# Performance work log

Measured on AMD Instinct MI355X. Metric: run time of the kernel, lower is better.

Reference implementation:

```python
import jax, jax.numpy as jnp
import numpy as np

EPS = 1e-7


def setup_inputs() -> dict:
    key = jax.random.key(0)
    k1, k2, k3 = jax.random.split(key, 3)
    N = 4194304
    risk_scores = jax.random.normal(k1, (N,), dtype=jnp.float32)
    times = jax.random.randint(k2, (N,), 0, 50000, dtype=jnp.int32)
    events = jax.random.randint(k3, (N,), 0, 2, dtype=jnp.int32)
    return {"risk_scores": risk_scores, "times": times, "events": events}


def _efron_loss(risk_scores, times, events):
    N = risk_scores.shape[0]
    # sort descending by time (stable), as in torch.argsort(times, descending=True)
    order = jnp.argsort(-times, stable=True)
    lr = risk_scores[order]          # log risk, sorted
    t = times[order]
    e = events[order]
    risk = jnp.exp(lr)
    # reversed cumsum: risk set sum for each position (suffix sum)
    csr = jnp.cumsum(risk[::-1])[::-1]
    m = (e == 1)
    mf = m.astype(lr.dtype)
    # segment id per unique time value (contiguous after sort)
    boundary = jnp.concatenate([jnp.zeros((1,), jnp.int32),
                                (t[1:] != t[:-1]).astype(jnp.int32)])
    seg = jnp.cumsum(boundary)       # [N] in [0, N)
    idx = jnp.arange(N)
    # per-segment stats over events
    n_per_seg = jax.ops.segment_sum(mf, seg, num_segments=N)            # n_events at this time
    risk_at_seg = jax.ops.segment_sum(risk * mf, seg, num_segments=N)   # sum of exp(lr) over tied events
    first_ev = jax.ops.segment_min(jnp.where(m, idx, N), seg, num_segments=N)  # event_idx[0]
    seg_start = jax.ops.segment_min(idx, seg, num_segments=N)
    # within-tie event rank j (0-based): events in this segment strictly before i
    c_excl = jnp.cumsum(mf) - mf
    j = c_excl - c_excl[seg_start[seg]]
    n_i = n_per_seg[seg]
    risk_time_i = risk_at_seg[seg]
    risk_set_i = csr[jnp.clip(first_ev[seg], 0, N - 1)]
    correction = (j / jnp.maximum(n_i, 1.0)) * risk_time_i
    per_event = jnp.log(risk_set_i - correction + EPS) - lr
    total_loss = jnp.sum(jnp.where(m, per_event, 0.0))
    total_events = jnp.sum(mf)
    return jnp.where(total_events > 0, total_loss / jnp.maximum(total_events, 1.0), 0.0)


def reference(risk_scores, times, events):
    return _efron_loss(risk_scores, times, events)
```

## Files before the change

kernel.cpp:

```cpp
#include <hip/hip_runtime.h>
#include <math.h>

#define TBINS   50000
#define NR      5
#define RBINS   10000
#define GROUP   256
#define NGROUPS 196
#define EPSF    1e-7f
#define PTHR    1024
#define STRIDE  (PTHR * 8)
#define MAXNS   104
#define MAXNB   (NR * 128)

#define OFF_ALLG  0
#define OFF_EVG   200000
#define OFF_CNTG  400000
#define OFF_GSUM  600000
#define OFF_SCAL  600800
#define OFF_NEV   600816
#define OFF_LRP   600832
#define OFF_NP    603392
#define OFF_SLICE 605952
#define PER_SLICE 400000

__global__ __launch_bounds__(PTHR, 8) void k_pass(
        const float* __restrict__ lr, const int* __restrict__ tm,
        const int* __restrict__ ev, int N, int NS, int CH, char* ws) {
    __shared__ float    s_all[RBINS];
    __shared__ unsigned s_evcnt[RBINS];
    __shared__ float    red_f[16];
    __shared__ int      red_i[16];

    int bid = blockIdx.x;
    int range, slice;
    if ((NS & 7) == 0) {
        int x  = bid & 7;
        int q  = bid >> 3;
        range  = q % NR;
        slice  = (q / NR) * 8 + x;
    } else {
        range = bid % NR;
        slice = bid / NR;
    }
    int rbase = range * RBINS;
    int tid   = threadIdx.x;

    for (int i = tid; i < RBINS; i += PTHR) { s_all[i] = 0.f; s_evcnt[i] = 0u; }
    __syncthreads();

    float l_lr = 0.f;
    int   l_n  = 0;
    int begin = slice * CH;
    int end   = begin + CH; if (end > N) end = N;
    int span  = end - begin; if (span < 0) span = 0;
    int jmax  = span / STRIDE;

    const float* plr = lr + begin + tid * 8;
    const int*   ptm = tm + begin + tid * 8;
    const int*   pev = ev + begin + tid * 8;

#define PROC1(T, L, E) {                                                  \
        unsigned rel_ = (unsigned)((T) - rbase);                          \
        if (rel_ < (unsigned)RBINS) {                                     \
            float r_ = __expf(L);                                         \
            atomicAdd(&s_all[rel_], r_);                                  \
            if ((E) != 0) {                                               \
                l_lr += (L); l_n++;                                       \
                unsigned enc_ = (1u << 28) + (unsigned)(r_ * 65536.0f + 0.5f); \
                atomicAdd(&s_evcnt[rel_], enc_);                          \
            }                                                             \
        } }

#define PROC8(TA, TB, LA, LB, EA, EB)                                    \
        PROC1(TA.x, LA.x, EA.x) PROC1(TA.y, LA.y, EA.y)                  \
        PROC1(TA.z, LA.z, EA.z) PROC1(TA.w, LA.w, EA.w)                  \
        PROC1(TB.x, LB.x, EB.x) PROC1(TB.y, LB.y, EB.y)                  \
        PROC1(TB.z, LB.z, EB.z) PROC1(TB.w, LB.w, EB.w)

#define LOADSLOT(TA, TB, LA, LB, EA, EB, OFF)                            \
        TA = *(const int4*)(ptm + (OFF));   TB = *(const int4*)(ptm + (OFF) + 4); \
        LA = *(const float4*)(plr + (OFF)); LB = *(const float4*)(plr + (OFF) + 4); \
        EA = *(const int4*)(pev + (OFF));   EB = *(const int4*)(pev + (OFF) + 4);

    int4 ta0, tb0, ea0, eb0; float4 la0, lb0;
    int4 ta1, tb1, ea1, eb1; float4 la1, lb1;
    if (jmax > 0) { LOADSLOT(ta0, tb0, la0, lb0, ea0, eb0, 0) }
    if (jmax > 1) { LOADSLOT(ta1, tb1, la1, lb1, ea1, eb1, STRIDE) }

    for (int j = 0; j < jmax; j += 2) {
        PROC8(ta0, tb0, la0, lb0, ea0, eb0)
        if (j + 2 < jmax) { int off = (j + 2) * STRIDE; LOADSLOT(ta0, tb0, la0, lb0, ea0, eb0, off) }
        if (j + 1 < jmax) {
            PROC8(ta1, tb1, la1, lb1, ea1, eb1)
            if (j + 3 < jmax) { int off = (j + 3) * STRIDE; LOADSLOT(ta1, tb1, la1, lb1, ea1, eb1, off) }
        }
    }
    for (int i = begin + jmax * STRIDE + tid; i < end; i += PTHR) {
        int T = tm[i]; float L = lr[i]; int E = ev[i];
        PROC1(T, L, E)
    }

    int lane = tid & 63, wv = tid >> 6;
    #pragma unroll
    for (int off = 32; off > 0; off >>= 1) {
        l_lr += __shfl_down(l_lr, off, 64);
        l_n  += __shfl_down(l_n,  off, 64);
    }
    if (lane == 0) { red_f[wv] = l_lr; red_i[wv] = l_n; }
    __syncthreads();
    if (tid == 0) {
        float s = 0.f; int c = 0;
        #pragma unroll
        for (int w = 0; w < 16; ++w) { s += red_f[w]; c += red_i[w]; }
        ((float*)(ws + OFF_LRP))[bid] = s;
        ((int*)(ws + OFF_NP))[bid]   = c;
    }

    float*    wa  = (float*)(ws + OFF_SLICE + (size_t)slice * PER_SLICE);
    unsigned* wec = (unsigned*)(ws + OFF_SLICE + (size_t)slice * PER_SLICE + (size_t)TBINS * 4);
    for (int i = tid; i < RBINS; i += PTHR) {
        wa[rbase + i]  = s_all[i];
        wec[rbase + i] = s_evcnt[i];
    }
}

__global__ __launch_bounds__(256) void k_reduce(char* ws, int NS, int NB,
                                                float* all_g, float* ev_g, int* cnt_g,
                                                float* gsum, double* scal, int* nev) {
    __shared__ float lds[4];
    __shared__ float ldsf2[4];
    __shared__ int   ldsi2[4];
    int tid = threadIdx.x;
    int b = blockIdx.x * 256 + tid;
    float a = 0.f, d = 0.f; int c = 0;
    if (b < TBINS) {
        const char* base = ws + OFF_SLICE;
        for (int s = 0; s < NS; ++s) {
            const float*    wa  = (const float*)(base + (size_t)s * PER_SLICE);
            const unsigned* wec = (const unsigned*)(base + (size_t)s * PER_SLICE + (size_t)TBINS * 4);
            a += wa[b];
            unsigned e = wec[b];
            c += (int)(e >> 28);
            d += (float)(e & 0x0FFFFFFFu) * (1.0f / 65536.0f);
        }
        all_g[b] = a; ev_g[b] = d; cnt_g[b] = c;
    }
    int lane = tid & 63, wv = tid >> 6;
    float v = a;
    #pragma unroll
    for (int off = 32; off > 0; off >>= 1) v += __shfl_down(v, off, 64);
    if (lane == 0) lds[wv] = v;
    __syncthreads();
    if (tid == 0) {
        float s = 0.f;
        #pragma unroll
        for (int w = 0; w < 4; ++w) s += lds[w];
        gsum[blockIdx.x] = s;
    }

    if (blockIdx.x == 0) {
        float pl = 0.f; int pn = 0;
        for (int i = tid; i < NB; i += 256) {
            pl += ((const float*)(ws + OFF_LRP))[i];
            pn += ((const int*)(ws + OFF_NP))[i];
        }
        #pragma unroll
        for (int off = 32; off > 0; off >>= 1) {
            pl += __shfl_down(pl, off, 64);
            pn += __shfl_down(pn, off, 64);
        }
        if (lane == 0) { ldsf2[wv] = pl; ldsi2[wv] = pn; }
        __syncthreads();
        if (tid == 0) {
            float s = 0.f; int n = 0;
            #pragma unroll
            for (int w = 0; w < 4; ++w) { s += ldsf2[w]; n += ldsi2[w]; }
            scal[0] = (double)s;
            scal[1] = 0.0;
            *nev    = n;
        }
    }
}

__global__ __launch_bounds__(256) void k_loss(
        const float* __restrict__ all_g, const float* __restrict__ gsum,
        const int* __restrict__ cnt_g, const float* __restrict__ ev_g,
        double* scal) {
    __shared__ float lds_r[4];
    __shared__ float lds_s[4];
    __shared__ float sh_base;
    int b   = blockIdx.x;
    int tid = threadIdx.x;
    int t   = b * GROUP + tid;
    int lane = tid & 63, wv = tid >> 6;

    float gv = (tid < b) ? gsum[tid] : 0.f;
    float red = gv;
    #pragma unroll
    for (int off = 32; off > 0; off >>= 1) red += __shfl_down(red, off, 64);
    if (lane == 0) lds_r[wv] = red;
    __syncthreads();
    if (tid == 0) {
        float s = 0.f;
        #pragma unroll
        for (int w = 0; w < 4; ++w) s += lds_r[w];
        sh_base = s;
    }
    __syncthreads();
    float base = sh_base;

    float v = (t < TBINS) ? all_g[t] : 0.f;
    float x = v;
    #pragma unroll
    for (int off = 1; off < 64; off <<= 1) {
        float y = __shfl_up(x, off, 64);
        if (lane >= off) x += y;
    }
    if (lane == 63) lds_s[wv] = x;
    __syncthreads();
    float wbase = 0.f;
    for (int w = 0; w < wv; ++w) wbase += lds_s[w];
    float prefix = base + wbase + (x - v);

    float acc = 0.f;
    if (t < TBINS) {
        int n = cnt_g[t];
        if (n > 0) {
            float D  = ev_g[t];
            float nf = (float)n;
            float P  = D + (v - D) * (nf / (nf + 1.f));
            float R  = prefix + P;
            for (int j = 0; j < n; ++j) {
                float arg = R - ((float)j / nf) * D + EPSF;
                acc += __logf(arg);
            }
        }
    }
    __syncthreads();
    #pragma unroll
    for (int off = 32; off > 0; off >>= 1) acc += __shfl_down(acc, off, 64);
    if (lane == 0) lds_r[wv] = acc;
    __syncthreads();
    if (tid == 0) {
        float s = 0.f;
        #pragma unroll
        for (int w = 0; w < 4; ++w) s += lds_r[w];
        atomicAdd(&scal[1], (double)s);
    }
}

__global__ void k_final(const double* __restrict__ scal,
                        const int* __restrict__ nev, float* out) {
    if (threadIdx.x == 0 && blockIdx.x == 0) {
        int n = *nev;
        double loss = (n > 0) ? (scal[1] - scal[0]) / (double)n : 0.0;
        out[0] = (float)loss;
    }
}

extern "C" void kernel_launch(void* const* d_in, const int* in_sizes, int n_in,
                              void* d_out, int out_size, void* d_ws, size_t ws_size,
                              hipStream_t stream) {
    const float* lr = (const float*)d_in[0];
    const int*   tm = (const int*)d_in[1];
    const int*   ev = (const int*)d_in[2];
    int N = in_sizes[0];

    char*   ws    = (char*)d_ws;
    float*  all_g = (float*)(ws + OFF_ALLG);
    float*  ev_g  = (float*)(ws + OFF_EVG);
    int*    cnt_g = (int*)(ws + OFF_CNTG);
    float*  gsum  = (float*)(ws + OFF_GSUM);
    double* scal  = (double*)(ws + OFF_SCAL);
    int*    nev   = (int*)(ws + OFF_NEV);

    size_t avail = (ws_size > (size_t)OFF_SLICE) ? ws_size - OFF_SLICE : 0;
    int NS = (int)(avail / PER_SLICE);
    if (NS > MAXNS) NS = MAXNS;
    if (NS >= 8) NS &= ~7;
    if (NS < 1) NS = 1;
    int NB = NR * NS;
    int CH = (int)(((long long)N + (long long)NS * STRIDE - 1) / ((long long)NS * STRIDE)) * STRIDE;

    k_pass<<<NB, PTHR, 0, stream>>>(lr, tm, ev, N, NS, CH, ws);
    k_reduce<<<NGROUPS, 256, 0, stream>>>(ws, NS, NB, all_g, ev_g, cnt_g, gsum, scal, nev);
    k_loss<<<NGROUPS, 256, 0, stream>>>(all_g, gsum, cnt_g, ev_g, scal);
    k_final<<<1, 64, 0, stream>>>(scal, nev, (float*)d_out);
}
```

Measured before the change: 93.75 us.

## Pack time, half-precision risk and event flag into one word before histogramming

Adds a prep kernel that reads the three input arrays once, computes exp(lr), and packs the time (high 16 bits), an fp16 risk value and the event bit into one 32-bit word. It also reduces the event log-risk sums there. The histogram pass then rereads only the packed array across its range blocks, with 4 time ranges instead of 5 and at most 64 slices. This cuts redundant global reads and repeated exp work, at the cost of an extra kernel, a packed-array write, and fp16 rounding of risk values that may hurt accuracy.

```diff
diff --git a/kernel.cpp b/kernel.cpp
--- a/kernel.cpp
+++ b/kernel.cpp
@@ -1,16 +1,17 @@
 #include <hip/hip_runtime.h>
+#include <hip/hip_fp16.h>
 #include <math.h>
 
 #define TBINS   50000
-#define NR      5
-#define RBINS   10000
+#define NR      4
+#define RBINS   12500
 #define GROUP   256
 #define NGROUPS 196
 #define EPSF    1e-7f
 #define PTHR    1024
 #define STRIDE  (PTHR * 8)
-#define MAXNS   104
-#define MAXNB   (NR * 128)
+#define MAXNS   64
+#define NPREP   1024
 
 #define OFF_ALLG  0
 #define OFF_EVG   200000
@@ -19,112 +20,142 @@
 #define OFF_SCAL  600800
 #define OFF_NEV   600816
 #define OFF_LRP   600832
-#define OFF_NP    603392
-#define OFF_SLICE 605952
+#define OFF_NP    604928
+#define OFF_PACK  609024
 #define PER_SLICE 400000
 
-__global__ __launch_bounds__(PTHR, 8) void k_pass(
+__global__ __launch_bounds__(256) void k_prep(
         const float* __restrict__ lr, const int* __restrict__ tm,
-        const int* __restrict__ ev, int N, int NS, int CH, char* ws) {
+        const int* __restrict__ ev, int N, unsigned* __restrict__ packed,
+        float* lrp, int* np) {
+    __shared__ float red_f[4];
+    __shared__ int   red_i[4];
+    int tid = threadIdx.x;
+    int gid = blockIdx.x * 256 + tid;
+    const int T = NPREP * 256;
+    float l_lr = 0.f;
+    int   l_n  = 0;
+
+#define PACK1(L, TT, E, OUT) {                                            \
+        float r_ = __expf(L);                                             \
+        unsigned hb_ = (unsigned)__half_as_ushort(__float2half(r_));      \
+        if ((E) != 0) { hb_ |= 0x8000u; l_lr += (L); l_n++; }             \
+        OUT = ((unsigned)(TT) << 16) | hb_; }
+
+    int nvec = N & ~3;
+    for (int base = gid * 4; base < nvec; base += T * 4) {
+        float4 l4 = *(const float4*)(lr + base);
+        int4   t4 = *(const int4*)(tm + base);
+        int4   e4 = *(const int4*)(ev + base);
+        uint4 o;
+        PACK1(l4.x, t4.x, e4.x, o.x)
+        PACK1(l4.y, t4.y, e4.y, o.y)
+        PACK1(l4.z, t4.z, e4.z, o.z)
+        PACK1(l4.w, t4.w, e4.w, o.w)
+        *(uint4*)(packed + base) = o;
+    }
+    for (int i = nvec + gid; i < N; i += T) {
+        unsigned o;
+        PACK1(lr[i], tm[i], ev[i], o)
+        packed[i] = o;
+    }
+
+    int lane = tid & 63, wv = tid >> 6;
+    #pragma unroll
+    for (int off = 32; off > 0; off >>= 1) {
+        l_lr += __shfl_down(l_lr, off, 64);
+        l_n  += __shfl_down(l_n,  off, 64);
+    }
+    if (lane == 0) { red_f[wv] = l_lr; red_i[wv] = l_n; }
+    __syncthreads();
+    if (tid == 0) {
+        float s = 0.f; int c = 0;
+        #pragma unroll
+        for (int w = 0; w < 4; ++w) { s += red_f[w]; c += red_i[w]; }
+        lrp[blockIdx.x] = s;
+        np[blockIdx.x]  = c;
+    }
+}
+
+__global__ __launch_bounds__(PTHR) void k_pass(
+        const unsigned* __restrict__ packed, int N, int NS, int CH, char* slices) {
     __shared__ float    s_all[RBINS];
     __shared__ unsigned s_evcnt[RBINS];
-    __shared__ float    red_f[16];
-    __shared__ int      red_i[16];
 
     int bid = blockIdx.x;
     int range, slice;
     if ((NS & 7) == 0) {
         int x  = bid & 7;
         int q  = bid >> 3;
-        range  = q % NR;
-        slice  = (q / NR) * 8 + x;
+        range  = q & 3;
+        slice  = (q >> 2) * 8 + x;
     } else {
-        range = bid % NR;
-        slice = bid / NR;
-    }
-    int rbase = range * RBINS;
-    int tid   = threadIdx.x;
+        range = bid & 3;
+        slice = bid >> 2;
+    }
+    unsigned rbase = (unsigned)(range * RBINS);
+    int tid = threadIdx.x;
 
     for (int i = tid; i < RBINS; i += PTHR) { s_all[i] = 0.f; s_evcnt[i] = 0u; }
     __syncthreads();
 
-    float l_lr = 0.f;
-    int   l_n  = 0;
     int begin = slice * CH;
     int end   = begin + CH; if (end > N) end = N;
     int span  = end - begin; if (span < 0) span = 0;
     int jmax  = span / STRIDE;
 
-    const float* plr = lr + begin + tid * 8;
-    const int*   ptm = tm + begin + tid * 8;
-    const int*   pev = ev + begin + tid * 8;
-
-#define PROC1(T, L, E) {                                                  \
-        unsigned rel_ = (unsigned)((T) - rbase);                          \
+    const unsigned* pp = packed + begin + tid * 8;
+
+#define PROC1(P) {                                                        \
+        unsigned rel_ = ((P) >> 16) - rbase;                              \
         if (rel_ < (unsigned)RBINS) {                                     \
-            float r_ = __expf(L);                                         \
+            float r_ = __half2float(__ushort_as_half((unsigned short)((P) & 0x7FFFu))); \
             atomicAdd(&s_all[rel_], r_);                                  \
-            if ((E) != 0) {                                               \
-                l_lr += (L); l_n++;                                       \
+            if ((P) & 0x8000u) {                                          \
                 unsigned enc_ = (1u << 28) + (unsigned)(r_ * 65536.0f + 0.5f); \
                 atomicAdd(&s_evcnt[rel_], enc_);                          \
             }                                                             \
         } }
 
-#define PROC8(TA, TB, LA, LB, EA, EB)                                    \
-        PROC1(TA.x, LA.x, EA.x) PROC1(TA.y, LA.y, EA.y)                  \
-        PROC1(TA.z, LA.z, EA.z) PROC1(TA.w, LA.w, EA.w)                  \
-        PROC1(TB.x, LB.x, EB.x) PROC1(TB.y, LB.y, EB.y)                  \
-        PROC1(TB.z, LB.z, EB.z) PROC1(TB.w, LB.w, EB.w)
-
-#define LOADSLOT(TA, TB, LA, LB, EA, EB, OFF)                            \
-        TA = *(const int4*)(ptm + (OFF));   TB = *(const int4*)(ptm + (OFF) + 4); \
-        LA = *(const float4*)(plr + (OFF)); LB = *(const float4*)(plr + (OFF) + 4); \
-        EA = *(const int4*)(pev + (OFF));   EB = *(const int4*)(pev + (OFF) + 4);
-
-    int4 ta0, tb0, ea0, eb0; float4 la0, lb0;
-    int4 ta1, tb1, ea1, eb1; float4 la1, lb1;
-    if (jmax > 0) { LOADSLOT(ta0, tb0, la0, lb0, ea0, eb0, 0) }
-    if (jmax > 1) { LOADSLOT(ta1, tb1, la1, lb1, ea1, eb1, STRIDE) }
+#define PROC8(A, B)                                                      \
+        PROC1(A.x) PROC1(A.y) PROC1(A.z) PROC1(A.w)                      \
+        PROC1(B.x) PROC1(B.y) PROC1(B.z) PROC1(B.w)
+
+    uint4 a0, b0, a1, b1;
+    if (jmax > 0) { a0 = *(const uint4*)pp; b0 = *(const uint4*)(pp + 4); }
+    if (jmax > 1) { a1 = *(const uint4*)(pp + STRIDE); b1 = *(const uint4*)(pp + STRIDE + 4); }
 
     for (int j = 0; j < jmax; j += 2) {
-        PROC8(ta0, tb0, la0, lb0, ea0, eb0)
-        if (j + 2 < jmax) { int off = (j + 2) * STRIDE; LOADSLOT(ta0, tb0, la0, lb0, ea0, eb0, off) }
+        PROC8(a0, b0)
+        if (j + 2 < jmax) {
+            a0 = *(const uint4*)(pp + (j + 2) * STRIDE);
+            b0 = *(const uint4*)(pp + (j + 2) * STRIDE + 4);
+        }
         if (j + 1 < jmax) {
-            PROC8(ta1, tb1, la1, lb1, ea1, eb1)
-            if (j + 3 < jmax) { int off = (j + 3) * STRIDE; LOADSLOT(ta1, tb1, la1, lb1, ea1, eb1, off) }
+            PROC8(a1, b1)
+            if (j + 3 < jmax) {
+                a1 = *(const uint4*)(pp + (j + 3) * STRIDE);
+                b1 = *(const uint4*)(pp + (j + 3) * STRIDE + 4);
+            }
         }
     }
     for (int i = begin + jmax * STRIDE + tid; i < end; i += PTHR) {
-        int T = tm[i]; float L = lr[i]; int E = ev[i];
-        PROC1(T, L, E)
-    }
-
-    int lane = tid & 63, wv = tid >> 6;
-    #pragma unroll
-    for (int off = 32; off > 0; off >>= 1) {
-        l_lr += __shfl_down(l_lr, off, 64);
-        l_n  += __shfl_down(l_n,  off, 64);
-    }
-    if (lane == 0) { red_f[wv] = l_lr; red_i[wv] = l_n; }
-    __syncthreads();
-    if (tid == 0) {
-        float s = 0.f; int c = 0;
-        #pragma unroll
-        for (int w = 0; w < 16; ++w) { s += red_f[w]; c += red_i[w]; }
-        ((float*)(ws + OFF_LRP))[bid] = s;
-        ((int*)(ws + OFF_NP))[bid]   = c;
-    }
-
-    float*    wa  = (float*)(ws + OFF_SLICE + (size_t)slice * PER_SLICE);
-    unsigned* wec = (unsigned*)(ws + OFF_SLICE + (size_t)slice * PER_SLICE + (size_t)TBINS * 4);
+        unsigned P = packed[i];
+        PROC1(P)
+    }
+    __syncthreads();
+
+    float*    wa  = (float*)(slices + (size_t)slice * PER_SLICE);
+    unsigned* wec = (unsigned*)(slices + (size_t)slice * PER_SLICE + (size_t)TBINS * 4);
     for (int i = tid; i < RBINS; i += PTHR) {
         wa[rbase + i]  = s_all[i];
         wec[rbase + i] = s_evcnt[i];
     }
 }
 
-__global__ __launch_bounds__(256) void k_reduce(char* ws, int NS, int NB,
+__global__ __launch_bounds__(256) void k_reduce(const char* __restrict__ slices, int NS,
+                                                const float* __restrict__ lrp,
+                                                const int* __restrict__ np,
                                                 float* all_g, float* ev_g, int* cnt_g,
                                                 float* gsum, double* scal, int* nev) {
     __shared__ float lds[4];
@@ -134,10 +165,9 @@
     int b = blockIdx.x * 256 + tid;
     float a = 0.f, d = 0.f; int c = 0;
     if (b < TBINS) {
-        const char* base = ws + OFF_SLICE;
         for (int s = 0; s < NS; ++s) {
-            const float*    wa  = (const float*)(base + (size_t)s * PER_SLICE);
-            const unsigned* wec = (const unsigned*)(base + (size_t)s * PER_SLICE + (size_t)TBINS * 4);
+            const float*    wa  = (const float*)(slices + (size_t)s * PER_SLICE);
+            const unsigned* wec = (const unsigned*)(slices + (size_t)s * PER_SLICE + (size_t)TBINS * 4);
             a += wa[b];
             unsigned e = wec[b];
             c += (int)(e >> 28);
@@ -160,10 +190,7 @@
 
     if (blockIdx.x == 0) {
         float pl = 0.f; int pn = 0;
-        for (int i = tid; i < NB; i += 256) {
-            pl += ((const float*)(ws + OFF_LRP))[i];
-            pn += ((const int*)(ws + OFF_NP))[i];
-        }
+        for (int i = tid; i < NPREP; i += 256) { pl += lrp[i]; pn += np[i]; }
         #pragma unroll
         for (int off = 32; off > 0; off >>= 1) {
             pl += __shfl_down(pl, off, 64);
@@ -266,15 +293,21 @@
     const int*   ev = (const int*)d_in[2];
     int N = in_sizes[0];
 
-    char*   ws    = (char*)d_ws;
-    float*  all_g = (float*)(ws + OFF_ALLG);
-    float*  ev_g  = (float*)(ws + OFF_EVG);
-    int*    cnt_g = (int*)(ws + OFF_CNTG);
-    float*  gsum  = (float*)(ws + OFF_GSUM);
-    double* scal  = (double*)(ws + OFF_SCAL);
-    int*    nev   = (int*)(ws + OFF_NEV);
-
-    size_t avail = (ws_size > (size_t)OFF_SLICE) ? ws_size - OFF_SLICE : 0;
+    char*     ws     = (char*)d_ws;
+    float*    all_g  = (float*)(ws + OFF_ALLG);
+    float*    ev_g   = (float*)(ws + OFF_EVG);
+    int*      cnt_g  = (int*)(ws + OFF_CNTG);
+    float*    gsum   = (float*)(ws + OFF_GSUM);
+    double*   scal   = (double*)(ws + OFF_SCAL);
+    int*      nev    = (int*)(ws + OFF_NEV);
+    float*    lrp    = (float*)(ws + OFF_LRP);
+    int*      np     = (int*)(ws + OFF_NP);
+    unsigned* packed = (unsigned*)(ws + OFF_PACK);
+
+    size_t off_slice = ((size_t)OFF_PACK + (size_t)N * 4 + 255) & ~(size_t)255;
+    char*  slices    = ws + off_slice;
+
+    size_t avail = (ws_size > off_slice) ? ws_size - off_slice : 0;
     int NS = (int)(avail / PER_SLICE);
     if (NS > MAXNS) NS = MAXNS;
     if (NS >= 8) NS &= ~7;
@@ -282,8 +315,9 @@
     int NB = NR * NS;
     int CH = (int)(((long long)N + (long long)NS * STRIDE - 1) / ((long long)NS * STRIDE)) * STRIDE;
 
-    k_pass<<<NB, PTHR, 0, stream>>>(lr, tm, ev, N, NS, CH, ws);
-    k_reduce<<<NGROUPS, 256, 0, stream>>>(ws, NS, NB, all_g, ev_g, cnt_g, gsum, scal, nev);
+    k_prep<<<NPREP, 256, 0, stream>>>(lr, tm, ev, N, packed, lrp, np);
+    k_pass<<<NB, PTHR, 0, stream>>>(packed, N, NS, CH, slices);
+    k_reduce<<<NGROUPS, 256, 0, stream>>>(slices, NS, lrp, np, all_g, ev_g, cnt_g, gsum, scal, nev);
     k_loss<<<NGROUPS, 256, 0, stream>>>(all_g, gsum, cnt_g, ev_g, scal);
     k_final<<<1, 64, 0, stream>>>(scal, nev, (float*)d_out);
 }
```

After: 78.92 us. 15.8% less time.

## Partition inputs by time range into packed fp16 records before LDS histogramming

Applied to the files above, without the earlier changes.

Adds a partition kernel that computes exp(lr), packs time, an fp16 risk value and the event flag into 32-bit records, and scatters them into per-wave buckets for four time ranges using ballot/popcount compaction. The histogram kernel then reads only its own range's records instead of every block rescanning the full input, and stores slice partials as packed fp16 pairs plus byte counts. The slice count is fixed at 64, which shrinks the cross-slice reduction. The final kernel is folded into k_loss through a last-block ticket. In exchange the partition output is an extra global write and read, and fp16 rounding of the risk values and partials reduces accuracy, with some risk of overflow for large exp values.

```diff
diff --git a/kernel.cpp b/kernel.cpp
--- a/kernel.cpp
+++ b/kernel.cpp
@@ -1,132 +1,165 @@
 #include <hip/hip_runtime.h>
+#include <hip/hip_fp16.h>
 #include <math.h>
 
 #define TBINS   50000
-#define NR      5
-#define RBINS   10000
+#define NR      4
+#define RBINS   12500
 #define GROUP   256
 #define NGROUPS 196
 #define EPSF    1e-7f
-#define PTHR    1024
-#define STRIDE  (PTHR * 8)
-#define MAXNS   104
-#define MAXNB   (NR * 128)
-
-#define OFF_ALLG  0
-#define OFF_EVG   200000
-#define OFF_CNTG  400000
-#define OFF_GSUM  600000
-#define OFF_SCAL  600800
-#define OFF_NEV   600816
-#define OFF_LRP   600832
-#define OFF_NP    603392
-#define OFF_SLICE 605952
-#define PER_SLICE 400000
-
-__global__ __launch_bounds__(PTHR, 8) void k_pass(
+#define NPB     256
+#define NWV     16
+#define NSL     64
+#define PER_SLICE 256000
+
+#define OFF_SCAL  0
+#define OFF_NEV   16
+#define OFF_DONE  20
+#define OFF_GSUM  64
+#define OFF_ALLG  2048
+#define OFF_EVG   202048
+#define OFF_CNTG  402048
+#define OFF_LRP   602048
+#define OFF_NP    603072
+#define OFF_CNTS  604160
+#define OFF_PART  669696
+
+__global__ __launch_bounds__(1024) void k_part(
         const float* __restrict__ lr, const int* __restrict__ tm,
-        const int* __restrict__ ev, int N, int NS, int CH, char* ws) {
-    __shared__ float    s_all[RBINS];
-    __shared__ unsigned s_evcnt[RBINS];
-    __shared__ float    red_f[16];
-    __shared__ int      red_i[16];
-
-    int bid = blockIdx.x;
-    int range, slice;
-    if ((NS & 7) == 0) {
-        int x  = bid & 7;
-        int q  = bid >> 3;
-        range  = q % NR;
-        slice  = (q / NR) * 8 + x;
-    } else {
-        range = bid % NR;
-        slice = bid / NR;
-    }
-    int rbase = range * RBINS;
-    int tid   = threadIdx.x;
-
-    for (int i = tid; i < RBINS; i += PTHR) { s_all[i] = 0.f; s_evcnt[i] = 0u; }
-    __syncthreads();
-
-    float l_lr = 0.f;
-    int   l_n  = 0;
-    int begin = slice * CH;
-    int end   = begin + CH; if (end > N) end = N;
-    int span  = end - begin; if (span < 0) span = 0;
-    int jmax  = span / STRIDE;
-
-    const float* plr = lr + begin + tid * 8;
-    const int*   ptm = tm + begin + tid * 8;
-    const int*   pev = ev + begin + tid * 8;
-
-#define PROC1(T, L, E) {                                                  \
-        unsigned rel_ = (unsigned)((T) - rbase);                          \
-        if (rel_ < (unsigned)RBINS) {                                     \
-            float r_ = __expf(L);                                         \
-            atomicAdd(&s_all[rel_], r_);                                  \
-            if ((E) != 0) {                                               \
-                l_lr += (L); l_n++;                                       \
-                unsigned enc_ = (1u << 28) + (unsigned)(r_ * 65536.0f + 0.5f); \
-                atomicAdd(&s_evcnt[rel_], enc_);                          \
-            }                                                             \
-        } }
-
-#define PROC8(TA, TB, LA, LB, EA, EB)                                    \
-        PROC1(TA.x, LA.x, EA.x) PROC1(TA.y, LA.y, EA.y)                  \
-        PROC1(TA.z, LA.z, EA.z) PROC1(TA.w, LA.w, EA.w)                  \
-        PROC1(TB.x, LB.x, EB.x) PROC1(TB.y, LB.y, EB.y)                  \
-        PROC1(TB.z, LB.z, EB.z) PROC1(TB.w, LB.w, EB.w)
-
-#define LOADSLOT(TA, TB, LA, LB, EA, EB, OFF)                            \
-        TA = *(const int4*)(ptm + (OFF));   TB = *(const int4*)(ptm + (OFF) + 4); \
-        LA = *(const float4*)(plr + (OFF)); LB = *(const float4*)(plr + (OFF) + 4); \
-        EA = *(const int4*)(pev + (OFF));   EB = *(const int4*)(pev + (OFF) + 4);
-
-    int4 ta0, tb0, ea0, eb0; float4 la0, lb0;
-    int4 ta1, tb1, ea1, eb1; float4 la1, lb1;
-    if (jmax > 0) { LOADSLOT(ta0, tb0, la0, lb0, ea0, eb0, 0) }
-    if (jmax > 1) { LOADSLOT(ta1, tb1, la1, lb1, ea1, eb1, STRIDE) }
-
-    for (int j = 0; j < jmax; j += 2) {
-        PROC8(ta0, tb0, la0, lb0, ea0, eb0)
-        if (j + 2 < jmax) { int off = (j + 2) * STRIDE; LOADSLOT(ta0, tb0, la0, lb0, ea0, eb0, off) }
-        if (j + 1 < jmax) {
-            PROC8(ta1, tb1, la1, lb1, ea1, eb1)
-            if (j + 3 < jmax) { int off = (j + 3) * STRIDE; LOADSLOT(ta1, tb1, la1, lb1, ea1, eb1, off) }
-        }
-    }
-    for (int i = begin + jmax * STRIDE + tid; i < end; i += PTHR) {
-        int T = tm[i]; float L = lr[i]; int E = ev[i];
-        PROC1(T, L, E)
-    }
-
-    int lane = tid & 63, wv = tid >> 6;
+        const int* __restrict__ ev, int N, int WCH,
+        unsigned* __restrict__ part, unsigned* __restrict__ cnts,
+        float* __restrict__ lrp, int* __restrict__ np) {
+    __shared__ float red_f[16];
+    __shared__ int   red_i[16];
+    const int b = blockIdx.x, tid = threadIdx.x;
+    const int w = tid >> 6, lane = tid & 63;
+    const unsigned long long lmask = (1ULL << lane) - 1ULL;
+
+    const int base0 = (b * NWV + w) * WCH;
+    const unsigned seg0 = (unsigned)(b * NWV + w) * 4u;
+    unsigned wc0 = 0, wc1 = 0, wc2 = 0, wc3 = 0;
+    float l_lr = 0.f; int l_n = 0;
+
+#define PART1(L, T, E, VALID) {                                           \
+        float r_ = __expf(L);                                             \
+        unsigned hb_ = (unsigned)__half_as_ushort(__float2half(r_));      \
+        bool ve_ = (VALID) && ((E) != 0);                                 \
+        if (ve_) { hb_ |= 0x8000u; l_lr += (L); l_n++; }                  \
+        unsigned P_  = ((unsigned)(T) << 16) | hb_;                       \
+        unsigned rg_ = ((unsigned)(T)) / 12500u;                          \
+        { unsigned long long m_ = __ballot((VALID) && rg_ == 0u);         \
+          if ((VALID) && rg_ == 0u)                                       \
+              part[(size_t)(seg0 + 0u) * WCH + wc0 + (unsigned)__popcll(m_ & lmask)] = P_; \
+          wc0 += (unsigned)__popcll(m_); }                                \
+        { unsigned long long m_ = __ballot((VALID) && rg_ == 1u);         \
+          if ((VALID) && rg_ == 1u)                                       \
+              part[(size_t)(seg0 + 1u) * WCH + wc1 + (unsigned)__popcll(m_ & lmask)] = P_; \
+          wc1 += (unsigned)__popcll(m_); }                                \
+        { unsigned long long m_ = __ballot((VALID) && rg_ == 2u);         \
+          if ((VALID) && rg_ == 2u)                                       \
+              part[(size_t)(seg0 + 2u) * WCH + wc2 + (unsigned)__popcll(m_ & lmask)] = P_; \
+          wc2 += (unsigned)__popcll(m_); }                                \
+        { unsigned long long m_ = __ballot((VALID) && rg_ == 3u);         \
+          if ((VALID) && rg_ == 3u)                                       \
+              part[(size_t)(seg0 + 3u) * WCH + wc3 + (unsigned)__popcll(m_ & lmask)] = P_; \
+          wc3 += (unsigned)__popcll(m_); }                                \
+    }
+
+    for (int it = 0; it < WCH; it += 256) {
+        int idx = base0 + it + lane * 4;
+        float4 l4 = {0.f, 0.f, 0.f, 0.f};
+        int4   t4 = {0, 0, 0, 0};
+        int4   e4 = {0, 0, 0, 0};
+        if (idx + 3 < N) {
+            l4 = *(const float4*)(lr + idx);
+            t4 = *(const int4*)(tm + idx);
+            e4 = *(const int4*)(ev + idx);
+        } else if (idx < N) {
+            float* lp = (float*)&l4; int* tp = (int*)&t4; int* ep = (int*)&e4;
+            for (int k = 0; k < 4 && idx + k < N; ++k) {
+                lp[k] = lr[idx + k]; tp[k] = tm[idx + k]; ep[k] = ev[idx + k];
+            }
+        }
+        PART1(l4.x, t4.x, e4.x, (idx + 0) < N)
+        PART1(l4.y, t4.y, e4.y, (idx + 1) < N)
+        PART1(l4.z, t4.z, e4.z, (idx + 2) < N)
+        PART1(l4.w, t4.w, e4.w, (idx + 3) < N)
+    }
+
+    if (lane == 0) {
+        unsigned* c = cnts + seg0;
+        c[0] = wc0; c[1] = wc1; c[2] = wc2; c[3] = wc3;
+    }
+
     #pragma unroll
     for (int off = 32; off > 0; off >>= 1) {
         l_lr += __shfl_down(l_lr, off, 64);
         l_n  += __shfl_down(l_n,  off, 64);
     }
-    if (lane == 0) { red_f[wv] = l_lr; red_i[wv] = l_n; }
+    if (lane == 0) { red_f[w] = l_lr; red_i[w] = l_n; }
     __syncthreads();
     if (tid == 0) {
         float s = 0.f; int c = 0;
         #pragma unroll
-        for (int w = 0; w < 16; ++w) { s += red_f[w]; c += red_i[w]; }
-        ((float*)(ws + OFF_LRP))[bid] = s;
-        ((int*)(ws + OFF_NP))[bid]   = c;
-    }
-
-    float*    wa  = (float*)(ws + OFF_SLICE + (size_t)slice * PER_SLICE);
-    unsigned* wec = (unsigned*)(ws + OFF_SLICE + (size_t)slice * PER_SLICE + (size_t)TBINS * 4);
-    for (int i = tid; i < RBINS; i += PTHR) {
-        wa[rbase + i]  = s_all[i];
-        wec[rbase + i] = s_evcnt[i];
-    }
-}
-
-__global__ __launch_bounds__(256) void k_reduce(char* ws, int NS, int NB,
+        for (int i = 0; i < NWV; ++i) { s += red_f[i]; c += red_i[i]; }
+        lrp[b] = s; np[b] = c;
+    }
+}
+
+__global__ __launch_bounds__(1024) void k_pass(
+        const unsigned* __restrict__ part, const unsigned* __restrict__ cnts,
+        int WCH, char* __restrict__ slices) {
+    __shared__ float    s_all[RBINS];
+    __shared__ unsigned s_evcnt[RBINS];
+    const int bid = blockIdx.x;
+    const int r = bid & 3, s = bid >> 2;
+    const unsigned rbase = (unsigned)(r * RBINS);
+    const int tid = threadIdx.x, w = tid >> 6, lane = tid & 63;
+
+    for (int i = tid; i < RBINS; i += 1024) { s_all[i] = 0.f; s_evcnt[i] = 0u; }
+    __syncthreads();
+
+    for (int sl = w; sl < 4 * NWV; sl += NWV) {
+        int pb = 4 * s + (sl >> 4);
+        int pw = sl & 15;
+        unsigned seg = (unsigned)(pb * NWV + pw) * 4u + (unsigned)r;
+        unsigned cnt = cnts[seg];
+        const unsigned* sp = part + (size_t)seg * WCH;
+        for (unsigned i = (unsigned)lane; i < cnt; i += 64u) {
+            unsigned P = sp[i];
+            unsigned rel = (P >> 16) - rbase;
+            if (rel < (unsigned)RBINS) {
+                float r_ = __half2float(__ushort_as_half((unsigned short)(P & 0x7FFFu)));
+                atomicAdd(&s_all[rel], r_);
+                if (P & 0x8000u) {
+                    unsigned enc = (1u << 28) + (unsigned)(r_ * 65536.0f + 0.5f);
+                    atomicAdd(&s_evcnt[rel], enc);
+                }
+            }
+        }
+    }
+    __syncthreads();
+
+    char* sb = slices + (size_t)s * PER_SLICE;
+    unsigned*      wab = (unsigned*)sb;
+    unsigned char* wcq = (unsigned char*)(sb + 200000);
+    for (int i = tid; i < RBINS; i += 1024) {
+        float a = s_all[i];
+        unsigned ec = s_evcnt[i];
+        float e = (float)(ec & 0x0FFFFFFFu) * (1.0f / 65536.0f);
+        wab[rbase + i] = (unsigned)__half_as_ushort(__float2half(a))
+                       | ((unsigned)__half_as_ushort(__float2half(e)) << 16);
+        wcq[rbase + i] = (unsigned char)(ec >> 28);
+    }
+}
+
+__global__ __launch_bounds__(256) void k_reduce(const char* __restrict__ slices,
+                                                const float* __restrict__ lrp,
+                                                const int* __restrict__ np,
                                                 float* all_g, float* ev_g, int* cnt_g,
-                                                float* gsum, double* scal, int* nev) {
+                                                float* gsum, double* scal, int* nev,
+                                                int* done) {
     __shared__ float lds[4];
     __shared__ float ldsf2[4];
     __shared__ int   ldsi2[4];
@@ -134,14 +167,12 @@
     int b = blockIdx.x * 256 + tid;
     float a = 0.f, d = 0.f; int c = 0;
     if (b < TBINS) {
-        const char* base = ws + OFF_SLICE;
-        for (int s = 0; s < NS; ++s) {
-            const float*    wa  = (const float*)(base + (size_t)s * PER_SLICE);
-            const unsigned* wec = (const unsigned*)(base + (size_t)s * PER_SLICE + (size_t)TBINS * 4);
-            a += wa[b];
-            unsigned e = wec[b];
-            c += (int)(e >> 28);
-            d += (float)(e & 0x0FFFFFFFu) * (1.0f / 65536.0f);
+        for (int s = 0; s < NSL; ++s) {
+            const char* sb = slices + (size_t)s * PER_SLICE;
+            unsigned ab = ((const unsigned*)sb)[b];
+            a += __half2float(__ushort_as_half((unsigned short)(ab & 0xFFFFu)));
+            d += __half2float(__ushort_as_half((unsigned short)(ab >> 16)));
+            c += ((const unsigned char*)(sb + 200000))[b];
         }
         all_g[b] = a; ev_g[b] = d; cnt_g[b] = c;
     }
@@ -159,11 +190,8 @@
     }
 
     if (blockIdx.x == 0) {
-        float pl = 0.f; int pn = 0;
-        for (int i = tid; i < NB; i += 256) {
-            pl += ((const float*)(ws + OFF_LRP))[i];
-            pn += ((const int*)(ws + OFF_NP))[i];
-        }
+        float pl = lrp[tid];
+        int   pn = np[tid];
         #pragma unroll
         for (int off = 32; off > 0; off >>= 1) {
             pl += __shfl_down(pl, off, 64);
@@ -178,6 +206,7 @@
             scal[0] = (double)s;
             scal[1] = 0.0;
             *nev    = n;
+            *done   = 0;
         }
     }
 }
@@ -185,7 +214,8 @@
 __global__ __launch_bounds__(256) void k_loss(
         const float* __restrict__ all_g, const float* __restrict__ gsum,
         const int* __restrict__ cnt_g, const float* __restrict__ ev_g,
-        double* scal) {
+        double* scal, const int* __restrict__ nev, int* done,
+        float* __restrict__ out) {
     __shared__ float lds_r[4];
     __shared__ float lds_s[4];
     __shared__ float sh_base;
@@ -218,9 +248,9 @@
     }
     if (lane == 63) lds_s[wv] = x;
     __syncthreads();
-    float wbase = 0.f;
-    for (int w = 0; w < wv; ++w) wbase += lds_s[w];
-    float prefix = base + wbase + (x - v);
+    float wb = 0.f;
+    for (int w = 0; w < wv; ++w) wb += lds_s[w];
+    float prefix = base + wb + (x - v);
 
     float acc = 0.f;
     if (t < TBINS) {
@@ -246,15 +276,13 @@
         #pragma unroll
         for (int w = 0; w < 4; ++w) s += lds_r[w];
         atomicAdd(&scal[1], (double)s);
-    }
-}
-
-__global__ void k_final(const double* __restrict__ scal,
-                        const int* __restrict__ nev, float* out) {
-    if (threadIdx.x == 0 && blockIdx.x == 0) {
-        int n = *nev;
-        double loss = (n > 0) ? (scal[1] - scal[0]) / (double)n : 0.0;
-        out[0] = (float)loss;
+        __threadfence();
+        int ticket = atomicAdd(done, 1);
+        if (ticket == NGROUPS - 1) {
+            double logsum = atomicAdd(&scal[1], 0.0);
+            int n = *nev;
+            out[0] = (n > 0) ? (float)((logsum - scal[0]) / (double)n) : 0.f;
+        }
     }
 }
 
@@ -266,24 +294,27 @@
     const int*   ev = (const int*)d_in[2];
     int N = in_sizes[0];
 
-    char*   ws    = (char*)d_ws;
-    float*  all_g = (float*)(ws + OFF_ALLG);
-    float*  ev_g  = (float*)(ws + OFF_EVG);
-    int*    cnt_g = (int*)(ws + OFF_CNTG);
-    float*  gsum  = (float*)(ws + OFF_GSUM);
-    double* scal  = (double*)(ws + OFF_SCAL);
-    int*    nev   = (int*)(ws + OFF_NEV);
-
-    size_t avail = (ws_size > (size_t)OFF_SLICE) ? ws_size - OFF_SLICE : 0;
-    int NS = (int)(avail / PER_SLICE);
-    if (NS > MAXNS) NS = MAXNS;
-    if (NS >= 8) NS &= ~7;
-    if (NS < 1) NS = 1;
-    int NB = NR * NS;
-    int CH = (int)(((long long)N + (long long)NS * STRIDE - 1) / ((long long)NS * STRIDE)) * STRIDE;
-
-    k_pass<<<NB, PTHR, 0, stream>>>(lr, tm, ev, N, NS, CH, ws);
-    k_reduce<<<NGROUPS, 256, 0, stream>>>(ws, NS, NB, all_g, ev_g, cnt_g, gsum, scal, nev);
-    k_loss<<<NGROUPS, 256, 0, stream>>>(all_g, gsum, cnt_g, ev_g, scal);
-    k_final<<<1, 64, 0, stream>>>(scal, nev, (float*)d_out);
-}
+    char*     ws    = (char*)d_ws;
+    double*   scal  = (double*)(ws + OFF_SCAL);
+    int*      nev   = (int*)(ws + OFF_NEV);
+    int*      done  = (int*)(ws + OFF_DONE);
+    float*    gsum  = (float*)(ws + OFF_GSUM);
+    float*    all_g = (float*)(ws + OFF_ALLG);
+    float*    ev_g  = (float*)(ws + OFF_EVG);
+    int*      cnt_g = (int*)(ws + OFF_CNTG);
+    float*    lrp   = (float*)(ws + OFF_LRP);
+    int*      np    = (int*)(ws + OFF_NP);
+    unsigned* cnts  = (unsigned*)(ws + OFF_CNTS);
+    unsigned* part  = (unsigned*)(ws + OFF_PART);
+
+    int WCH = (int)((((long long)N + (NPB * NWV) - 1) / (NPB * NWV) + 255) / 256) * 256;
+    size_t part_bytes = (size_t)NPB * NWV * 4 * WCH * 4;
+    char* slices = ws + OFF_PART + part_bytes;
+
+    k_part<<<NPB, 1024, 0, stream>>>(lr, tm, ev, N, WCH, part, cnts, lrp, np);
+    k_pass<<<NR * NSL, 1024, 0, stream>>>(part, cnts, WCH, slices);
+    k_reduce<<<NGROUPS, 256, 0, stream>>>(slices, lrp, np, all_g, ev_g, cnt_g,
+                                          gsum, scal, nev, done);
+    k_loss<<<NGROUPS, 256, 0, stream>>>(all_g, gsum, cnt_g, ev_g, scal, nev, done,
+                                        (float*)d_out);
+}
```

Measured after the change: 75.14 us (median of 2 runs). -19.9%, faster.
